# Kernel optimization log

Measured on AMD Instinct MI355X. Metric: run time of the kernel, lower is better.

Reference implementation:

```python
import jax, jax.numpy as jnp
import numpy as np

BATCH, LENGTH, IN, STATE, OUT = 8, 4096, 512, 256, 512


def setup_inputs() -> dict:
    key = jax.random.key(0)
    k1, k2, k3, k4, k5 = jax.random.split(key, 5)
    u = jax.random.normal(k1, (BATCH, LENGTH, IN), dtype=jnp.float32)
    x0 = jax.random.normal(k2, (BATCH, STATE), dtype=jnp.float32)
    A = 0.9999 * (2.0 * jax.random.uniform(k3, (STATE,), dtype=jnp.float32) - 1.0)
    B = jax.random.normal(k4, (IN, STATE), dtype=jnp.float32) / (STATE + IN) ** 0.5
    C = jax.random.normal(k5, (STATE, OUT), dtype=jnp.float32) / STATE ** 0.5
    return {"u": u, "x0": x0, "A": A, "B": B, "C": C}


def reference(u, x0, A, B, C):
    L = u.shape[1]
    # A_powers[t, n] = A[n] ** t, shape [L, state]
    A_powers = jnp.power(A[None, :], jnp.arange(L, dtype=u.dtype)[:, None])
    uB = u @ B  # [batch, L, state]
    # FFT convolution; inputs are real so rfft/irfft gives same result as
    # real(ifft(fft*fft)) in the original.
    T = 2 ** int(np.ceil(np.log2(2 * L - 1)))
    Af = jnp.fft.rfft(A_powers, n=T, axis=0)  # [T/2+1, state]
    Uf = jnp.fft.rfft(uB, n=T, axis=1)        # [batch, T/2+1, state]
    x = jnp.fft.irfft(Af[None, :, :] * Uf, n=T, axis=1)[:, :L]  # [batch, L, state]
    # initial-state contribution: A * A_powers * x0
    x = x + A[None, None, :] * A_powers[None, :, :] * x0[:, None, :]
    y = x @ C  # [batch, L, out]
    return (y, x[:, -1])
```

## Files before the change

kernel.cpp:

```cpp
#include <hip/hip_runtime.h>

#define BATCH   8
#define LENGTH  4096
#define IN_DIM  512
#define STATE   256
#define OUT_DIM 512
#define NC      256
#define LC      16

typedef __attribute__((ext_vector_type(8))) short bf16x8;
typedef __attribute__((ext_vector_type(4))) float f32x4;

union FragU { bf16x8 v; unsigned u[4]; };

__device__ __forceinline__ unsigned short bf16_rne(float v) {
    unsigned u = __builtin_bit_cast(unsigned, v);
    unsigned r = (u + 0x7FFFu + ((u >> 16) & 1u)) >> 16;
    return (unsigned short)r;
}
__device__ __forceinline__ float bf16_f(unsigned short h) {
    unsigned u = ((unsigned)h) << 16;
    return __builtin_bit_cast(float, u);
}

__global__ __launch_bounds__(256) void split_weights(
    const float* __restrict__ B, const float* __restrict__ C,
    unsigned short* __restrict__ Bhi, unsigned short* __restrict__ Blo,
    unsigned short* __restrict__ Chi, unsigned short* __restrict__ Clo)
{
    int id = blockIdx.x * 256 + threadIdx.x;
    if (id < IN_DIM * STATE) {
        int k = id & (IN_DIM - 1), n = id >> 9;
        float v = B[(size_t)k * STATE + n];
        unsigned short h = bf16_rne(v);
        Bhi[id] = h;
        Blo[id] = bf16_rne(v - bf16_f(h));
    } else {
        int id2 = id - IN_DIM * STATE;
        int k = id2 & (STATE - 1), n = id2 >> 8;
        float v = C[(size_t)k * OUT_DIM + n];
        unsigned short h = bf16_rne(v);
        Chi[id2] = h;
        Clo[id2] = bf16_rne(v - bf16_f(h));
    }
}

__global__ __launch_bounds__(512, 4) void gemm_dbuf(
    const float* __restrict__ Af, const unsigned short* __restrict__ Bthi,
    const unsigned short* __restrict__ Btlo, float* __restrict__ Cc,
    const float* __restrict__ Av, float* __restrict__ carry,
    int N_, int K)
{
    __shared__ unsigned short lds[2 * 16384];

    const int tid  = threadIdx.x;
    const int wave = tid >> 6;
    const int lane = tid & 63;
    const int n0 = blockIdx.x * 128;
    const int m0 = blockIdx.y * 128;

    const char* gp[4];
    int ldsoff[4], gstep[4];
    #pragma unroll
    for (int t = 0; t < 4; ++t) {
        int gi = wave * 4 + t;
        if (gi < 16) {
            int p = gi * 64 + lane;
            int row = p >> 3, s = p & 7;
            int l = s ^ (row & 7);
            gp[t] = (const char*)(Af + (size_t)(m0 + row) * K + l * 4);
            gstep[t] = 32 * 4;
            ldsoff[t] = gi * 512;
        } else {
            int q2 = (gi - 16) >> 3;
            int pi = gi & 7;
            int p = pi * 64 + lane;
            int row = p >> 2, s = p & 3;
            int l = s ^ ((row >> 1) & 3);
            const unsigned short* base = q2 ? Btlo : Bthi;
            gp[t] = (const char*)(base + (size_t)(n0 + row) * K + l * 8);
            gstep[t] = 32 * 2;
            ldsoff[t] = 8192 + q2 * 4096 + pi * 512;
        }
    }

    const int r = lane & 15, q = lane >> 4;
    const int wm = (wave >> 1) * 32, wn = (wave & 1) * 64;

    int aoff[2][2], boff[4];
    #pragma unroll
    for (int i = 0; i < 2; ++i) {
        int row = wm + i * 16 + r;
        #pragma unroll
        for (int h = 0; h < 2; ++h)
            aoff[i][h] = row * 64 + ((2 * q + h) ^ (row & 7)) * 8;
    }
    #pragma unroll
    for (int j = 0; j < 4; ++j) {
        int row = wn + j * 16 + r;
        boff[j] = row * 32 + (q ^ ((row >> 1) & 3)) * 8;
    }

    f32x4 acc[2][4];
    #pragma unroll
    for (int i = 0; i < 2; ++i)
        #pragma unroll
        for (int j = 0; j < 4; ++j)
            acc[i][j] = (f32x4){0.f, 0.f, 0.f, 0.f};

    #pragma unroll
    for (int t = 0; t < 4; ++t) {
        __builtin_amdgcn_global_load_lds(
            (const __attribute__((address_space(1))) unsigned*)(gp[t]),
            (__attribute__((address_space(3))) unsigned*)(&lds[ldsoff[t]]),
            16, 0, 0);
        gp[t] += gstep[t];
    }

    const int nit = K >> 5;
    for (int it = 0; it < nit; ++it) {
        asm volatile("" ::: "memory");
        __builtin_amdgcn_s_barrier();
        asm volatile("" ::: "memory");
        if (it + 1 < nit) {
            const int bb = ((it + 1) & 1) * 16384;
            #pragma unroll
            for (int t = 0; t < 4; ++t) {
                __builtin_amdgcn_global_load_lds(
                    (const __attribute__((address_space(1))) unsigned*)(gp[t]),
                    (__attribute__((address_space(3))) unsigned*)(&lds[bb + ldsoff[t]]),
                    16, 0, 0);
                gp[t] += gstep[t];
            }
            __builtin_amdgcn_s_waitcnt(0x0F74);
        } else {
            __builtin_amdgcn_s_waitcnt(0x0F70);
        }
        asm volatile("" ::: "memory");
        __builtin_amdgcn_s_barrier();
        asm volatile("" ::: "memory");

        const unsigned short* buf = &lds[(it & 1) * 16384];

        FragU ahi[2], alo[2];
        #pragma unroll
        for (int i = 0; i < 2; ++i) {
            #pragma unroll
            for (int h = 0; h < 2; ++h) {
                float4 f = *(const float4*)(buf + aoff[i][h]);
                unsigned bx = __builtin_bit_cast(unsigned, f.x);
                unsigned by = __builtin_bit_cast(unsigned, f.y);
                unsigned bz = __builtin_bit_cast(unsigned, f.z);
                unsigned bw = __builtin_bit_cast(unsigned, f.w);
                ahi[i].u[h * 2]     = __builtin_amdgcn_perm(by, bx, 0x07060302);
                ahi[i].u[h * 2 + 1] = __builtin_amdgcn_perm(bw, bz, 0x07060302);
                float lx = f.x - __builtin_bit_cast(float, bx & 0xFFFF0000u);
                float ly = f.y - __builtin_bit_cast(float, by & 0xFFFF0000u);
                float lz = f.z - __builtin_bit_cast(float, bz & 0xFFFF0000u);
                float lw = f.w - __builtin_bit_cast(float, bw & 0xFFFF0000u);
                alo[i].u[h * 2]     = __builtin_amdgcn_perm(
                    __builtin_bit_cast(unsigned, ly), __builtin_bit_cast(unsigned, lx), 0x07060302);
                alo[i].u[h * 2 + 1] = __builtin_amdgcn_perm(
                    __builtin_bit_cast(unsigned, lw), __builtin_bit_cast(unsigned, lz), 0x07060302);
            }
        }
        FragU bhi[4], blo[4];
        #pragma unroll
        for (int j = 0; j < 4; ++j) {
            bhi[j].v = *(const bf16x8*)(buf +  8192 + boff[j]);
            blo[j].v = *(const bf16x8*)(buf + 12288 + boff[j]);
        }
        #pragma unroll
        for (int i = 0; i < 2; ++i)
            #pragma unroll
            for (int j = 0; j < 4; ++j) {
                acc[i][j] = __builtin_amdgcn_mfma_f32_16x16x32_bf16(ahi[i].v, bhi[j].v, acc[i][j], 0, 0, 0);
                acc[i][j] = __builtin_amdgcn_mfma_f32_16x16x32_bf16(alo[i].v, bhi[j].v, acc[i][j], 0, 0, 0);
                acc[i][j] = __builtin_amdgcn_mfma_f32_16x16x32_bf16(ahi[i].v, blo[j].v, acc[i][j], 0, 0, 0);
            }
    }

    #pragma unroll
    for (int i = 0; i < 2; ++i) {
        #pragma unroll
        for (int reg = 0; reg < 4; ++reg) {
            int mg = m0 + wm + i * 16 + q * 4 + reg;
            float* dst = Cc + (size_t)mg * N_ + n0 + wn + r;
            dst[0]  = acc[i][0][reg];
            dst[16] = acc[i][1][reg];
            dst[32] = acc[i][2][reg];
            dst[48] = acc[i][3][reg];
        }
    }

    {
        const int b  = m0 >> 12;
        const int c0 = ((m0 & 4095) + wm) >> 4;
        #pragma unroll
        for (int j = 0; j < 4; ++j) {
            const int n = n0 + wn + j * 16 + r;
            const float a  = Av[n];
            const float a2 = a * a, a3 = a2 * a, a4 = a2 * a2;
            const float a8 = a4 * a4, a12 = a8 * a4;
            const float base = (q == 0) ? a12 : (q == 1) ? a8 : (q == 2) ? a4 : 1.f;
            #pragma unroll
            for (int i = 0; i < 2; ++i) {
                float partial = base * (a3 * acc[i][j][0] + a2 * acc[i][j][1]
                                      + a  * acc[i][j][2] +      acc[i][j][3]);
                partial += __shfl_xor(partial, 16);
                partial += __shfl_xor(partial, 32);
                if (q == 0)
                    carry[((size_t)b * NC + (c0 + i)) * STATE + n] = partial;
            }
        }
    }
}

__global__ __launch_bounds__(256) void scan_entries(
    const float* __restrict__ carry, const float* __restrict__ A,
    const float* __restrict__ x0, float* __restrict__ entry,
    float* __restrict__ x_last)
{
    const int b = blockIdx.x;
    const int n = threadIdx.x;
    const float a = A[n];
    float aL = a;
    #pragma unroll
    for (int k = 0; k < 4; ++k) aL *= aL;

    float s = x0[(size_t)b * STATE + n];
    const float* cr = carry + (size_t)b * NC * STATE + n;
    float* en = entry + (size_t)b * NC * STATE + n;
    #pragma unroll 16
    for (int c = 0; c < NC; ++c) {
        en[(size_t)c * STATE] = s;
        s = fmaf(aL, s, cr[(size_t)c * STATE]);
    }
    x_last[(size_t)b * STATE + n] = s;
}

__global__ __launch_bounds__(512, 4) void gemm_scan_apply(
    const float* __restrict__ uB, const unsigned short* __restrict__ Bthi,
    const unsigned short* __restrict__ Btlo, const float* __restrict__ Av,
    const float* __restrict__ entry, float* __restrict__ Cc,
    int N_, int K)
{
    __shared__ unsigned short lds[2 * 16384];

    const int tid  = threadIdx.x;
    const int wave = tid >> 6;
    const int lane = tid & 63;
    const int n0 = blockIdx.x * 128;
    const int m0 = blockIdx.y * 128;
    const int bb_ = m0 >> 12;
    const int c0_ = (m0 & 4095) >> 4;

    const char* gp[4];
    int ldsoff[4], gstep[4];
    #pragma unroll
    for (int t = 0; t < 4; ++t) {
        int gi = wave * 4 + t;
        if (gi < 16) {
            int p = gi * 64 + lane;
            int row = p >> 3, s = p & 7;
            int l = s ^ (row & 7);
            gp[t] = (const char*)(uB + (size_t)(m0 + row) * K + l * 4);
            gstep[t] = 32 * 4;
            ldsoff[t] = gi * 512;
        } else {
            int q2 = (gi - 16) >> 3;
            int pi = gi & 7;
            int p = pi * 64 + lane;
            int row = p >> 2, s = p & 3;
            int l = s ^ ((row >> 1) & 3);
            const unsigned short* base = q2 ? Btlo : Bthi;
            gp[t] = (const char*)(base + (size_t)(n0 + row) * K + l * 8);
            gstep[t] = 32 * 2;
            ldsoff[t] = 8192 + q2 * 4096 + pi * 512;
        }
    }

    const int r = lane & 15, q = lane >> 4;
    const int wm = (wave >> 1) * 32, wn = (wave & 1) * 64;

    int aoff[2][2], boff[4];
    #pragma unroll
    for (int i = 0; i < 2; ++i) {
        int row = wm + i * 16 + r;
        #pragma unroll
        for (int h = 0; h < 2; ++h)
            aoff[i][h] = row * 64 + ((2 * q + h) ^ (row & 7)) * 8;
    }
    #pragma unroll
    for (int j = 0; j < 4; ++j) {
        int row = wn + j * 16 + r;
        boff[j] = row * 32 + (q ^ ((row >> 1) & 3)) * 8;
    }

    const int sc = tid >> 5;
    const int sk = tid & 31;

    f32x4 acc[2][4];
    #pragma unroll
    for (int i = 0; i < 2; ++i)
        #pragma unroll
        for (int j = 0; j < 4; ++j)
            acc[i][j] = (f32x4){0.f, 0.f, 0.f, 0.f};

    #pragma unroll
    for (int t = 0; t < 4; ++t) {
        __builtin_amdgcn_global_load_lds(
            (const __attribute__((address_space(1))) unsigned*)(gp[t]),
            (__attribute__((address_space(3))) unsigned*)(&lds[ldsoff[t]]),
            16, 0, 0);
        gp[t] += gstep[t];
    }

    const int nit = K >> 5;
    for (int it = 0; it < nit; ++it) {
        asm volatile("" ::: "memory");
        __builtin_amdgcn_s_barrier();
        asm volatile("" ::: "memory");
        if (it + 1 < nit) {
            const int bb = ((it + 1) & 1) * 16384;
            #pragma unroll
            for (int t = 0; t < 4; ++t) {
                __builtin_amdgcn_global_load_lds(
                    (const __attribute__((address_space(1))) unsigned*)(gp[t]),
                    (__attribute__((address_space(3))) unsigned*)(&lds[bb + ldsoff[t]]),
                    16, 0, 0);
                gp[t] += gstep[t];
            }
            __builtin_amdgcn_s_waitcnt(0x0F74);
        } else {
            __builtin_amdgcn_s_waitcnt(0x0F70);
        }
        asm volatile("" ::: "memory");
        __builtin_amdgcn_s_barrier();
        asm volatile("" ::: "memory");

        unsigned short* bufw = &lds[(it & 1) * 16384];
        const unsigned short* buf = bufw;

        if (tid < 256) {
            const int kg = it * 32 + sk;
            const float a = Av[kg];
            float s = entry[((size_t)bb_ * NC + (c0_ + sc)) * STATE + kg];
            #pragma unroll
            for (int j = 0; j < 16; ++j) {
                int row = sc * 16 + j;
                int off = row * 64 + (((sk >> 2) ^ (row & 7)) * 8) + ((sk & 3) * 2);
                float v = *(const float*)(bufw + off);
                s = fmaf(a, s, v);
                *(float*)(bufw + off) = s;
            }
        }
        asm volatile("s_waitcnt lgkmcnt(0)" ::: "memory");
        __builtin_amdgcn_s_barrier();
        asm volatile("" ::: "memory");

        FragU ahi[2], alo[2];
        #pragma unroll
        for (int i = 0; i < 2; ++i) {
            #pragma unroll
            for (int h = 0; h < 2; ++h) {
                float4 f = *(const float4*)(buf + aoff[i][h]);
                unsigned bx = __builtin_bit_cast(unsigned, f.x);
                unsigned by = __builtin_bit_cast(unsigned, f.y);
                unsigned bz = __builtin_bit_cast(unsigned, f.z);
                unsigned bw = __builtin_bit_cast(unsigned, f.w);
                ahi[i].u[h * 2]     = __builtin_amdgcn_perm(by, bx, 0x07060302);
                ahi[i].u[h * 2 + 1] = __builtin_amdgcn_perm(bw, bz, 0x07060302);
                float lx = f.x - __builtin_bit_cast(float, bx & 0xFFFF0000u);
                float ly = f.y - __builtin_bit_cast(float, by & 0xFFFF0000u);
                float lz = f.z - __builtin_bit_cast(float, bz & 0xFFFF0000u);
                float lw = f.w - __builtin_bit_cast(float, bw & 0xFFFF0000u);
                alo[i].u[h * 2]     = __builtin_amdgcn_perm(
                    __builtin_bit_cast(unsigned, ly), __builtin_bit_cast(unsigned, lx), 0x07060302);
                alo[i].u[h * 2 + 1] = __builtin_amdgcn_perm(
                    __builtin_bit_cast(unsigned, lw), __builtin_bit_cast(unsigned, lz), 0x07060302);
            }
        }
        FragU bhi[4], blo[4];
        #pragma unroll
        for (int j = 0; j < 4; ++j) {
            bhi[j].v = *(const bf16x8*)(buf +  8192 + boff[j]);
            blo[j].v = *(const bf16x8*)(buf + 12288 + boff[j]);
        }
        #pragma unroll
        for (int i = 0; i < 2; ++i)
            #pragma unroll
            for (int j = 0; j < 4; ++j) {
                acc[i][j] = __builtin_amdgcn_mfma_f32_16x16x32_bf16(ahi[i].v, bhi[j].v, acc[i][j], 0, 0, 0);
                acc[i][j] = __builtin_amdgcn_mfma_f32_16x16x32_bf16(alo[i].v, bhi[j].v, acc[i][j], 0, 0, 0);
                acc[i][j] = __builtin_amdgcn_mfma_f32_16x16x32_bf16(ahi[i].v, blo[j].v, acc[i][j], 0, 0, 0);
            }
    }

    #pragma unroll
    for (int i = 0; i < 2; ++i) {
        #pragma unroll
        for (int reg = 0; reg < 4; ++reg) {
            int mg = m0 + wm + i * 16 + q * 4 + reg;
            float* dst = Cc + (size_t)mg * N_ + n0 + wn + r;
            dst[0]  = acc[i][0][reg];
            dst[16] = acc[i][1][reg];
            dst[32] = acc[i][2][reg];
            dst[48] = acc[i][3][reg];
        }
    }
}

extern "C" void kernel_launch(void* const* d_in, const int* in_sizes, int n_in,
                              void* d_out, int out_size, void* d_ws, size_t ws_size,
                              hipStream_t stream)
{
    const float* u  = (const float*)d_in[0];
    const float* x0 = (const float*)d_in[1];
    const float* A  = (const float*)d_in[2];
    const float* B  = (const float*)d_in[3];
    const float* C  = (const float*)d_in[4];

    const size_t MB = 1024 * 1024;
    char* ws = (char*)d_ws;

    float* uB    = (float*)(ws);
    float* carry = (float*)(ws + 32 * MB);
    float* entry = (float*)(ws + 34 * MB);
    unsigned short* Bt_hi = (unsigned short*)(ws + 36 * MB);
    unsigned short* Bt_lo = (unsigned short*)(ws + 36 * MB + 256 * 1024);
    unsigned short* Ct_hi = (unsigned short*)(ws + 36 * MB + 512 * 1024);
    unsigned short* Ct_lo = (unsigned short*)(ws + 36 * MB + 768 * 1024);

    float* y      = (float*)d_out;
    float* x_last = y + (size_t)BATCH * LENGTH * OUT_DIM;

    const int M = BATCH * LENGTH;

    split_weights<<<dim3((IN_DIM * STATE + STATE * OUT_DIM) / 256), dim3(256), 0, stream>>>(
        B, C, Bt_hi, Bt_lo, Ct_hi, Ct_lo);

    gemm_dbuf<<<dim3(STATE / 128, M / 128), dim3(512), 0, stream>>>(
        u, Bt_hi, Bt_lo, uB, A, carry, STATE, IN_DIM);

    scan_entries<<<dim3(BATCH), dim3(256), 0, stream>>>(carry, A, x0, entry, x_last);

    gemm_scan_apply<<<dim3(OUT_DIM / 128, M / 128), dim3(512), 0, stream>>>(
        uB, Ct_hi, Ct_lo, A, entry, y, OUT_DIM, STATE);
}
```

Baseline: 194.6 us.

## Parallelize chunk-carry scan with two-level group decomposition

Replaces the single sequential scan over 256 chunk carries (8 blocks total) with a two-level scan. The first kernel reduces each group of 16 chunks to a group carry, and the second kernel combines preceding group carries with A^256 and writes per-chunk entries. This spreads the serial dependency chain across 128 blocks instead of 8, at the cost of an extra kernel launch and re-reading the carries.

```diff
diff --git a/kernel.cpp b/kernel.cpp
--- a/kernel.cpp
+++ b/kernel.cpp
@@ -216,27 +216,58 @@
     }
 }
 
-__global__ __launch_bounds__(256) void scan_entries(
+__global__ __launch_bounds__(256) void scan_gc(
     const float* __restrict__ carry, const float* __restrict__ A,
-    const float* __restrict__ x0, float* __restrict__ entry,
-    float* __restrict__ x_last)
-{
-    const int b = blockIdx.x;
-    const int n = threadIdx.x;
+    float* __restrict__ GC)
+{
+    const int b = blockIdx.x, g = blockIdx.y, n = threadIdx.x;
     const float a = A[n];
     float aL = a;
     #pragma unroll
     for (int k = 0; k < 4; ++k) aL *= aL;
 
-    float s = x0[(size_t)b * STATE + n];
-    const float* cr = carry + (size_t)b * NC * STATE + n;
-    float* en = entry + (size_t)b * NC * STATE + n;
-    #pragma unroll 16
-    for (int c = 0; c < NC; ++c) {
-        en[(size_t)c * STATE] = s;
-        s = fmaf(aL, s, cr[(size_t)c * STATE]);
-    }
-    x_last[(size_t)b * STATE + n] = s;
+    const float* cr = carry + ((size_t)b * NC + g * 16) * STATE + n;
+    float v[16];
+    #pragma unroll
+    for (int i = 0; i < 16; ++i) v[i] = cr[(size_t)i * STATE];
+    float s = 0.f;
+    #pragma unroll
+    for (int i = 0; i < 16; ++i) s = fmaf(aL, s, v[i]);
+    GC[((size_t)b * 16 + g) * STATE + n] = s;
+}
+
+__global__ __launch_bounds__(256) void scan_fix(
+    const float* __restrict__ carry, const float* __restrict__ GC,
+    const float* __restrict__ A, const float* __restrict__ x0,
+    float* __restrict__ entry, float* __restrict__ x_last)
+{
+    const int b = blockIdx.x, g = blockIdx.y, n = threadIdx.x;
+    const float a = A[n];
+    float aL = a;
+    #pragma unroll
+    for (int k = 0; k < 4; ++k) aL *= aL;
+    float aG = aL;
+    #pragma unroll
+    for (int k = 0; k < 4; ++k) aG *= aG;
+
+    const float* cr = carry + ((size_t)b * NC + g * 16) * STATE + n;
+    float v[16];
+    #pragma unroll
+    for (int i = 0; i < 16; ++i) v[i] = cr[(size_t)i * STATE];
+
+    float S = x0[(size_t)b * STATE + n];
+    const float* gc = GC + (size_t)b * 16 * STATE + n;
+    for (int gp = 0; gp < g; ++gp)
+        S = fmaf(aG, S, gc[(size_t)gp * STATE]);
+
+    float* en = entry + ((size_t)b * NC + g * 16) * STATE + n;
+    float s = S;
+    #pragma unroll
+    for (int i = 0; i < 16; ++i) {
+        en[(size_t)i * STATE] = s;
+        s = fmaf(aL, s, v[i]);
+    }
+    if (g == 15) x_last[(size_t)b * STATE + n] = s;
 }
 
 __global__ __launch_bounds__(512, 4) void gemm_scan_apply(
@@ -427,10 +458,11 @@
     float* uB    = (float*)(ws);
     float* carry = (float*)(ws + 32 * MB);
     float* entry = (float*)(ws + 34 * MB);
-    unsigned short* Bt_hi = (unsigned short*)(ws + 36 * MB);
-    unsigned short* Bt_lo = (unsigned short*)(ws + 36 * MB + 256 * 1024);
-    unsigned short* Ct_hi = (unsigned short*)(ws + 36 * MB + 512 * 1024);
-    unsigned short* Ct_lo = (unsigned short*)(ws + 36 * MB + 768 * 1024);
+    float* GC    = (float*)(ws + 36 * MB);
+    unsigned short* Bt_hi = (unsigned short*)(ws + 36 * MB + 128 * 1024);
+    unsigned short* Bt_lo = (unsigned short*)(ws + 36 * MB + 384 * 1024);
+    unsigned short* Ct_hi = (unsigned short*)(ws + 36 * MB + 640 * 1024);
+    unsigned short* Ct_lo = (unsigned short*)(ws + 36 * MB + 896 * 1024);
 
     float* y      = (float*)d_out;
     float* x_last = y + (size_t)BATCH * LENGTH * OUT_DIM;
@@ -443,7 +475,8 @@
     gemm_dbuf<<<dim3(STATE / 128, M / 128), dim3(512), 0, stream>>>(
         u, Bt_hi, Bt_lo, uB, A, carry, STATE, IN_DIM);
 
-    scan_entries<<<dim3(BATCH), dim3(256), 0, stream>>>(carry, A, x0, entry, x_last);
+    scan_gc <<<dim3(BATCH, 16), dim3(256), 0, stream>>>(carry, A, GC);
+    scan_fix<<<dim3(BATCH, 16), dim3(256), 0, stream>>>(carry, GC, A, x0, entry, x_last);
 
     gemm_scan_apply<<<dim3(OUT_DIM / 128, M / 128), dim3(512), 0, stream>>>(
         uB, Ct_hi, Ct_lo, A, entry, y, OUT_DIM, STATE);
```

Measured after the change: 189.4 us. 1.03x faster.
